# Kernel optimization log

Hardware: AMD Instinct MI355X
Metric: run time of the kernel (lower is better)

Reference implementation:

```python
import jax, jax.numpy as jnp
import numpy as np

N_NODES = 50000
N_EDGES = 800000
N_GRAPHS = 64
FEAT = 125
POS = 3
CONV = 256
LIN = 256
OUT = 10


def _glorot(key, shape):
    fan_in, fan_out = shape[1], shape[0]
    lim = jnp.sqrt(6.0 / (fan_in + fan_out))
    return jax.random.uniform(key, shape, jnp.float32, -lim, lim)


def setup_inputs() -> dict:
    key = jax.random.key(0)
    ks = jax.random.split(key, 16)
    x = jax.random.normal(ks[0], (N_NODES, FEAT), jnp.float32)
    pos = jax.random.normal(ks[1], (N_NODES, POS), jnp.float32)
    edge_index = jax.random.randint(ks[2], (2, N_EDGES), 0, N_NODES, jnp.int64)
    batch = jnp.sort(jax.random.randint(ks[3], (N_NODES,), 0, N_GRAPHS, jnp.int64))
    in0 = FEAT + POS  # 128
    inp = {
        'x': x, 'pos': pos, 'edge_index': edge_index, 'batch': batch,
        'Wl0': _glorot(ks[4], (CONV, in0)), 'bl0': jnp.zeros((CONV,), jnp.float32), 'Wr0': _glorot(ks[5], (CONV, in0)),
        'Wl1': _glorot(ks[6], (CONV, CONV)), 'bl1': jnp.zeros((CONV,), jnp.float32), 'Wr1': _glorot(ks[7], (CONV, CONV)),
        'Wl2': _glorot(ks[8], (CONV, CONV)), 'bl2': jnp.zeros((CONV,), jnp.float32), 'Wr2': _glorot(ks[9], (CONV, CONV)),
        'lin_W': _glorot(ks[10], (LIN, CONV)), 'lin_b': jnp.zeros((LIN,), jnp.float32),
        'out_W': _glorot(ks[11], (OUT, LIN)), 'out_b': jnp.zeros((OUT,), jnp.float32),
    }
    return inp


def _sage_conv(x, src, dst, Wl, bl, Wr):
    # PyG SAGEConv (aggr='mean'): out = lin_l(mean_{j in N(i)} x_j) + lin_r(x_i)
    n = x.shape[0]
    s = jax.ops.segment_sum(x[src], dst, num_segments=n)            # [N, F]
    cnt = jax.ops.segment_sum(jnp.ones((src.shape[0], 1), x.dtype), dst, num_segments=n)
    agg = s / jnp.maximum(cnt, 1.0)
    return agg @ Wl.T + bl + x @ Wr.T


def reference(x, pos, edge_index, batch, Wl0, bl0, Wr0, Wl1, bl1, Wr1,
              Wl2, bl2, Wr2, lin_W, lin_b, out_W, out_b):
    src, dst = edge_index[0], edge_index[1]
    h = jnp.concatenate([x, pos], axis=1)                           # [N, 128]
    for Wl, bl, Wr in ((Wl0, bl0, Wr0), (Wl1, bl1, Wr1), (Wl2, bl2, Wr2)):
        h = jax.nn.relu(_sage_conv(h, src, dst, Wl, bl, Wr))
    g = jax.ops.segment_max(h, batch, num_segments=N_GRAPHS)        # [G, 256] global_max_pool
    g = g @ lin_W.T + lin_b
    return g @ out_W.T + out_b                                      # [G, 10]
```

## Files before the change

kernel.cpp:

```cpp
#include <hip/hip_runtime.h>
#include <hip/hip_bf16.h>

#define N_NODES 50000
#define N_EDGES 800000
#define N_GRAPHS 64
#define SCAN_BLK 98

typedef __attribute__((ext_vector_type(8))) short bf16x8;
typedef __attribute__((ext_vector_type(4))) float f32x4;

#define AS1 __attribute__((address_space(1)))
#define AS3 __attribute__((address_space(3)))

__device__ __forceinline__ float bf2f(ushort u) { return __uint_as_float(((unsigned)u) << 16); }
__device__ __forceinline__ ushort f2bf(float f) {
    unsigned b = __float_as_uint(f);
    b += 0x7fffu + ((b >> 16) & 1u);
    return (ushort)(b >> 16);
}

__device__ __forceinline__ void gl_lds16(const ushort* g, ushort* l) {
    __builtin_amdgcn_global_load_lds((const AS1 void*)g, (AS3 void*)l, 16, 0, 0);
}

__global__ void build_h0(const float* __restrict__ x, const float* __restrict__ pos,
                         ushort* __restrict__ h0, int n) {
    const size_t total = (size_t)n * 128;
    for (size_t idx = (size_t)blockIdx.x * blockDim.x + threadIdx.x; idx < total;
         idx += (size_t)gridDim.x * blockDim.x) {
        int i = (int)(idx >> 7);
        int j = (int)(idx & 127);
        float v = (j < 125) ? x[(size_t)i * 125 + j] : pos[(size_t)i * 3 + (j - 125)];
        h0[idx] = f2bf(v);
    }
}

__global__ void convert_weights(const float* __restrict__ w0, const float* __restrict__ w1,
                                const float* __restrict__ w2, const float* __restrict__ w3,
                                const float* __restrict__ w4, const float* __restrict__ w5,
                                ushort* __restrict__ o) {
    const int total = 32768 * 2 + 65536 * 4;
    for (int i = blockIdx.x * blockDim.x + threadIdx.x; i < total; i += gridDim.x * blockDim.x) {
        float v;
        if (i < 32768) v = w0[i];
        else if (i < 65536) v = w1[i - 32768];
        else {
            int j = i - 65536;
            int m = j >> 16;
            int r = j & 65535;
            v = (m == 0) ? w2[r] : (m == 1) ? w3[r] : (m == 2) ? w4[r] : w5[r];
        }
        o[i] = f2bf(v);
    }
}

__global__ void hist_dst(const int* __restrict__ dst, int* __restrict__ deg, int e) {
    for (int i = blockIdx.x * blockDim.x + threadIdx.x; i < e; i += gridDim.x * blockDim.x)
        atomicAdd(&deg[dst[i]], 1);
}

__global__ __launch_bounds__(256) void scan_k1(const int* __restrict__ deg,
                                               int* __restrict__ bsum, int n) {
    const int b = blockIdx.x, t = threadIdx.x;
    const int j = b * 512 + t * 2;
    int x = (j < n) ? deg[j] : 0;
    int y = (j + 1 < n) ? deg[j + 1] : 0;
    __shared__ int sm[256];
    sm[t] = x + y;
    __syncthreads();
    for (int st = 1; st < 256; st <<= 1) {
        int v = (t >= st) ? sm[t - st] : 0;
        __syncthreads();
        sm[t] += v;
        __syncthreads();
    }
    if (t == 255) bsum[b] = sm[255];
}

__global__ __launch_bounds__(128) void scan_k2(const int* __restrict__ bsum,
                                               int* __restrict__ bpre, int* __restrict__ off_n,
                                               int nb) {
    const int t = threadIdx.x;
    const int v = (t < nb) ? bsum[t] : 0;
    __shared__ int sm[128];
    sm[t] = v;
    __syncthreads();
    for (int st = 1; st < 128; st <<= 1) {
        int u = (t >= st) ? sm[t - st] : 0;
        __syncthreads();
        sm[t] += u;
        __syncthreads();
    }
    if (t < nb) bpre[t] = sm[t] - v;
    if (t == 127) off_n[0] = sm[127];
}

__global__ __launch_bounds__(256) void scan_k3(const int* __restrict__ deg,
                                               const int* __restrict__ bpre,
                                               int* __restrict__ off, int* __restrict__ cur,
                                               int n) {
    const int b = blockIdx.x, t = threadIdx.x;
    const int j = b * 512 + t * 2;
    int x = (j < n) ? deg[j] : 0;
    int y = (j + 1 < n) ? deg[j + 1] : 0;
    const int s = x + y;
    __shared__ int sm[256];
    sm[t] = s;
    __syncthreads();
    for (int st = 1; st < 256; st <<= 1) {
        int u = (t >= st) ? sm[t - st] : 0;
        __syncthreads();
        sm[t] += u;
        __syncthreads();
    }
    const int v0 = bpre[b] + sm[t] - s;
    if (j < n) { off[j] = v0; cur[j] = v0; }
    if (j + 1 < n) { off[j + 1] = v0 + x; cur[j + 1] = v0 + x; }
}

__global__ __launch_bounds__(256) void fill_csr(const int* __restrict__ src,
                                                const int* __restrict__ dst,
                                                int* __restrict__ cur,
                                                ushort* __restrict__ csr, int e) {
    const int g = blockIdx.x & 7;
    const int bid = blockIdx.x >> 3;
    const int nb = gridDim.x >> 3;
    const int lo = g * (N_NODES / 8), hi = lo + (N_NODES / 8);
    for (int i = bid * blockDim.x + threadIdx.x; i < e; i += nb * blockDim.x) {
        const int d = dst[i];
        if (d >= lo && d < hi) {
            int pos = atomicAdd(&cur[d], 1);
            csr[pos] = (ushort)src[i];
        }
    }
}

template <int F>
__global__ __launch_bounds__(256) void csr_mean(const ushort* __restrict__ h,
                                                const int* __restrict__ off,
                                                const ushort* __restrict__ idx,
                                                ushort* __restrict__ s, int n) {
    const int node = blockIdx.x * 4 + (threadIdx.x >> 6);
    if (node >= n) return;
    const int lane = threadIdx.x & 63;
    constexpr int LPR = F / 8;
    constexpr int EPW = 64 / LPR;
    const int sub = lane / LPR;
    const int l = lane % LPR;
    const int b = off[node];
    const int cnt = off[node + 1] - b;

    float s0[8] = {}, s1[8] = {}, s2[8] = {}, s3[8] = {};
    const ushort* hl = h + (size_t)l * 8;
    int q = sub;
    for (; q + 3 * EPW < cnt; q += 4 * EPW) {
        int i0 = idx[b + q];
        int i1 = idx[b + q + EPW];
        int i2 = idx[b + q + 2 * EPW];
        int i3 = idx[b + q + 3 * EPW];
        bf16x8 v0 = *(const bf16x8*)(hl + (size_t)i0 * F);
        bf16x8 v1 = *(const bf16x8*)(hl + (size_t)i1 * F);
        bf16x8 v2 = *(const bf16x8*)(hl + (size_t)i2 * F);
        bf16x8 v3 = *(const bf16x8*)(hl + (size_t)i3 * F);
#pragma unroll
        for (int j = 0; j < 8; ++j) s0[j] += bf2f((ushort)v0[j]);
#pragma unroll
        for (int j = 0; j < 8; ++j) s1[j] += bf2f((ushort)v1[j]);
#pragma unroll
        for (int j = 0; j < 8; ++j) s2[j] += bf2f((ushort)v2[j]);
#pragma unroll
        for (int j = 0; j < 8; ++j) s3[j] += bf2f((ushort)v3[j]);
    }
    for (; q < cnt; q += EPW) {
        int i0 = idx[b + q];
        bf16x8 v0 = *(const bf16x8*)(hl + (size_t)i0 * F);
#pragma unroll
        for (int j = 0; j < 8; ++j) s0[j] += bf2f((ushort)v0[j]);
    }
    const float w = 1.0f / (float)max(cnt, 1);
    bf16x8 o;
#pragma unroll
    for (int j = 0; j < 8; ++j) {
        float a = (s0[j] + s1[j]) + (s2[j] + s3[j]);
        if constexpr (EPW == 4) a += __shfl_xor(a, 16);
        a += __shfl_xor(a, 32);
        o[j] = (short)f2bf(a * w);
    }
    if (sub == 0) *(bf16x8*)(s + (size_t)node * F + l * 8) = o;
}

__global__ __launch_bounds__(256, 3) void sage_gemm(
    const ushort* __restrict__ S, const ushort* __restrict__ H,
    const ushort* __restrict__ Wl, const ushort* __restrict__ Wr,
    const float* __restrict__ bias, ushort* __restrict__ O, int n, int F) {
    constexpr int BM = 128, BN = 128, BK = 64;
    __shared__ ushort As[BM * BK];
    __shared__ ushort Bs[BN * BK];
    const int row0 = blockIdx.x * BM;
    const int col0 = blockIdx.y * BN;
    const int tid = threadIdx.x;
    const int wid = tid >> 6;
    const int wr = wid >> 1;
    const int wc = wid & 1;
    const int lane = tid & 63;
    const int lr = lane & 15;
    const int lk = lane >> 4;
    const int lrow = lane >> 3;
    const int lgg = lane & 7;

    f32x4 acc[4][4] = {};

    const int Ktot = 2 * F;
    for (int kb = 0; kb < Ktot; kb += BK) {
        const bool left = (kb < F);
        const int kofs = left ? kb : kb - F;
        const ushort* __restrict__ Ab = left ? S : H;
        const ushort* __restrict__ Wb = left ? Wl : Wr;
#pragma unroll
        for (int p = 0; p < 4; ++p) {
            const int rb = (p * 4 + wid) * 8;
            const int r = rb + lrow;
            const int sg = (lgg ^ (r & 7)) << 3;
            const int gr = min(row0 + r, n - 1);
            gl_lds16(Ab + (size_t)gr * F + kofs + sg, &As[rb * 64]);
            gl_lds16(Wb + (size_t)(col0 + r) * F + kofs + sg, &Bs[rb * 64]);
        }
        __syncthreads();
#pragma unroll
        for (int kh = 0; kh < 2; ++kh) {
            bf16x8 af[4], bg[4];
            const int g = kh * 4 + lk;
#pragma unroll
            for (int m = 0; m < 4; ++m) {
                const int ra = wr * 64 + m * 16 + lr;
                af[m] = *(const bf16x8*)&As[ra * 64 + ((g ^ (ra & 7)) << 3)];
            }
#pragma unroll
            for (int q = 0; q < 4; ++q) {
                const int rb2 = wc * 64 + q * 16 + lr;
                bg[q] = *(const bf16x8*)&Bs[rb2 * 64 + ((g ^ (rb2 & 7)) << 3)];
            }
#pragma unroll
            for (int m = 0; m < 4; ++m)
#pragma unroll
                for (int q = 0; q < 4; ++q)
                    acc[m][q] =
                        __builtin_amdgcn_mfma_f32_16x16x32_bf16(af[m], bg[q], acc[m][q], 0, 0, 0);
        }
        __syncthreads();
    }
#pragma unroll
    for (int q = 0; q < 4; ++q) {
        const int col = col0 + wc * 64 + q * 16 + lr;
        const float bv = bias[col];
#pragma unroll
        for (int m = 0; m < 4; ++m) {
            const int row = row0 + wr * 64 + m * 16 + lk * 4;
#pragma unroll
            for (int j = 0; j < 4; ++j) {
                if (row + j < n)
                    O[(size_t)(row + j) * 256 + col] = f2bf(fmaxf(acc[m][q][j] + bv, 0.f));
            }
        }
    }
}

__global__ __launch_bounds__(256) void pool_max(const ushort* __restrict__ h,
                                                const int* __restrict__ batch,
                                                int* __restrict__ gpool, int n) {
    const int CHUNK = 32;
    const int wave = threadIdx.x >> 6;
    const int lane = threadIdx.x & 63;
    const int c0 = (blockIdx.x * 4 + wave) * CHUNK;
    if (c0 >= n) return;
    const int c1 = min(c0 + CHUNK, n);
    const int fb = lane * 4;
    float m0 = 0.f, m1 = 0.f, m2 = 0.f, m3 = 0.f;
    int g = batch[c0];
    for (int i = c0; i < c1; ++i) {
        const int bg = batch[i];
        if (bg != g) {
            int* gp = &gpool[g * 256 + fb];
            atomicMax(gp + 0, __float_as_int(m0));
            atomicMax(gp + 1, __float_as_int(m1));
            atomicMax(gp + 2, __float_as_int(m2));
            atomicMax(gp + 3, __float_as_int(m3));
            m0 = m1 = m2 = m3 = 0.f;
            g = bg;
        }
        const ushort4 v = *(const ushort4*)(h + (size_t)i * 256 + fb);
        m0 = fmaxf(m0, bf2f(v.x));
        m1 = fmaxf(m1, bf2f(v.y));
        m2 = fmaxf(m2, bf2f(v.z));
        m3 = fmaxf(m3, bf2f(v.w));
    }
    int* gp = &gpool[g * 256 + fb];
    atomicMax(gp + 0, __float_as_int(m0));
    atomicMax(gp + 1, __float_as_int(m1));
    atomicMax(gp + 2, __float_as_int(m2));
    atomicMax(gp + 3, __float_as_int(m3));
}

__global__ __launch_bounds__(256) void head_kernel(
    const float* __restrict__ gpool, const float* __restrict__ linW,
    const float* __restrict__ linb, const float* __restrict__ outW,
    const float* __restrict__ outb, float* __restrict__ out) {
    __shared__ float gin[256];
    __shared__ float gl[256];
    int g = blockIdx.x, t = threadIdx.x;
    gin[t] = gpool[g * 256 + t];
    __syncthreads();
    float acc = linb[t];
    const float* w = linW + (size_t)t * 256;
#pragma unroll 4
    for (int k = 0; k < 256; ++k) acc = fmaf(gin[k], w[k], acc);
    gl[t] = acc;
    __syncthreads();
    if (t < 160) {
        int o = t >> 4, s = t & 15;
        float p = 0.f;
        for (int k = s; k < 256; k += 16) p = fmaf(gl[k], outW[o * 256 + k], p);
        p += __shfl_down(p, 8, 16);
        p += __shfl_down(p, 4, 16);
        p += __shfl_down(p, 2, 16);
        p += __shfl_down(p, 1, 16);
        if (s == 0) out[g * 10 + o] = p + outb[o];
    }
}

extern "C" void kernel_launch(void* const* d_in, const int* in_sizes, int n_in,
                              void* d_out, int out_size, void* d_ws, size_t ws_size,
                              hipStream_t stream) {
    const float* x    = (const float*)d_in[0];
    const float* pos  = (const float*)d_in[1];
    const int* ei     = (const int*)d_in[2];
    const int* batch  = (const int*)d_in[3];
    const float* Wl0  = (const float*)d_in[4];
    const float* bl0  = (const float*)d_in[5];
    const float* Wr0  = (const float*)d_in[6];
    const float* Wl1  = (const float*)d_in[7];
    const float* bl1  = (const float*)d_in[8];
    const float* Wr1  = (const float*)d_in[9];
    const float* Wl2  = (const float*)d_in[10];
    const float* bl2  = (const float*)d_in[11];
    const float* Wr2  = (const float*)d_in[12];
    const float* linW = (const float*)d_in[13];
    const float* linb = (const float*)d_in[14];
    const float* outW = (const float*)d_in[15];
    const float* outb = (const float*)d_in[16];
    float* out = (float*)d_out;

    const int* src = ei;
    const int* dst = ei + N_EDGES;
    const int N = N_NODES, E = N_EDGES;

    ushort* hA   = (ushort*)d_ws;
    ushort* hB   = hA + (size_t)N * 256;
    ushort* Sg   = hB + (size_t)N * 256;
    ushort* Wb   = Sg + (size_t)N * 256;
    int* off     = (int*)(Wb + 327680);
    int* cur     = off + (N + 1);
    ushort* csr  = (ushort*)(cur + N);
    int* gpool   = (int*)(csr + E);
    int* deg     = gpool + 64 * 256;
    int* bsum    = deg + N;
    int* bpre    = bsum + 128;

    ushort* Wl0b = Wb;
    ushort* Wr0b = Wb + 32768;
    ushort* Wl1b = Wb + 65536;
    ushort* Wr1b = Wb + 65536 + 65536;
    ushort* Wl2b = Wb + 65536 + 2 * 65536;
    ushort* Wr2b = Wb + 65536 + 3 * 65536;

    build_h0<<<dim3(1024), dim3(256), 0, stream>>>(x, pos, hA, N);
    convert_weights<<<dim3(640), dim3(256), 0, stream>>>(Wl0, Wr0, Wl1, Wr1, Wl2, Wr2, Wb);

    hipMemsetAsync(deg, 0, (size_t)N * sizeof(int), stream);
    hist_dst<<<dim3(1024), dim3(256), 0, stream>>>(dst, deg, E);
    scan_k1<<<dim3(SCAN_BLK), dim3(256), 0, stream>>>(deg, bsum, N);
    scan_k2<<<dim3(1), dim3(128), 0, stream>>>(bsum, bpre, off + N, SCAN_BLK);
    scan_k3<<<dim3(SCAN_BLK), dim3(256), 0, stream>>>(deg, bpre, off, cur, N);
    fill_csr<<<dim3(768), dim3(256), 0, stream>>>(src, dst, cur, csr, E);

    const dim3 gemm_grid((N + 127) / 128, 2), blk(256);

    csr_mean<128><<<dim3((N + 3) / 4), blk, 0, stream>>>(hA, off, csr, Sg, N);
    sage_gemm<<<gemm_grid, blk, 0, stream>>>(Sg, hA, Wl0b, Wr0b, bl0, hB, N, 128);

    csr_mean<256><<<dim3((N + 3) / 4), blk, 0, stream>>>(hB, off, csr, Sg, N);
    sage_gemm<<<gemm_grid, blk, 0, stream>>>(Sg, hB, Wl1b, Wr1b, bl1, hA, N, 256);

    csr_mean<256><<<dim3((N + 3) / 4), blk, 0, stream>>>(hA, off, csr, Sg, N);
    sage_gemm<<<gemm_grid, blk, 0, stream>>>(Sg, hA, Wl2b, Wr2b, bl2, hB, N, 256);

    hipMemsetAsync(gpool, 0, (size_t)N_GRAPHS * 256 * sizeof(int), stream);
    pool_max<<<dim3((N + 127) / 128), blk, 0, stream>>>(hB, batch, gpool, N);
    head_kernel<<<dim3(N_GRAPHS), blk, 0, stream>>>((const float*)gpool, linW, linb, outW, outb,
                                                    out);
}
```

Baseline: 369.3 us.

## Unroll gather to 8 loads, partition degree histogram, template GEMM on F

The CSR mean aggregation now issues eight independent neighbor-row loads per iteration instead of four, to keep more memory requests in flight. The degree histogram splits blocks into eight groups that each handle atomics for one slice of node ids, aiming for better atomic locality, though every group rereads the whole dst array. The SAGE GEMM is templated on F so its K loop is fully unrolled at compile time. The extra accumulators raise register pressure in the gather kernel and may lower occupancy.

```diff
diff --git a/kernel.cpp b/kernel.cpp
--- a/kernel.cpp
+++ b/kernel.cpp
@@ -54,9 +54,16 @@
     }
 }
 
-__global__ void hist_dst(const int* __restrict__ dst, int* __restrict__ deg, int e) {
-    for (int i = blockIdx.x * blockDim.x + threadIdx.x; i < e; i += gridDim.x * blockDim.x)
-        atomicAdd(&deg[dst[i]], 1);
+__global__ __launch_bounds__(256) void hist_dst(const int* __restrict__ dst,
+                                                int* __restrict__ deg, int e) {
+    const int g = blockIdx.x & 7;
+    const int bid = blockIdx.x >> 3;
+    const int nb = gridDim.x >> 3;
+    const int lo = g * (N_NODES / 8), hi = lo + (N_NODES / 8);
+    for (int i = bid * blockDim.x + threadIdx.x; i < e; i += nb * blockDim.x) {
+        const int d = dst[i];
+        if (d >= lo && d < hi) atomicAdd(&deg[d], 1);
+    }
 }
 
 __global__ __launch_bounds__(256) void scan_k1(const int* __restrict__ deg,
@@ -150,38 +157,38 @@
     const int b = off[node];
     const int cnt = off[node + 1] - b;
 
-    float s0[8] = {}, s1[8] = {}, s2[8] = {}, s3[8] = {};
+    float acc[8][8] = {};
     const ushort* hl = h + (size_t)l * 8;
     int q = sub;
+    for (; q + 7 * EPW < cnt; q += 8 * EPW) {
+        bf16x8 v[8];
+#pragma unroll
+        for (int t = 0; t < 8; ++t) v[t] = *(const bf16x8*)(hl + (size_t)idx[b + q + t * EPW] * F);
+#pragma unroll
+        for (int t = 0; t < 8; ++t)
+#pragma unroll
+            for (int j = 0; j < 8; ++j) acc[t][j] += bf2f((ushort)v[t][j]);
+    }
     for (; q + 3 * EPW < cnt; q += 4 * EPW) {
-        int i0 = idx[b + q];
-        int i1 = idx[b + q + EPW];
-        int i2 = idx[b + q + 2 * EPW];
-        int i3 = idx[b + q + 3 * EPW];
-        bf16x8 v0 = *(const bf16x8*)(hl + (size_t)i0 * F);
-        bf16x8 v1 = *(const bf16x8*)(hl + (size_t)i1 * F);
-        bf16x8 v2 = *(const bf16x8*)(hl + (size_t)i2 * F);
-        bf16x8 v3 = *(const bf16x8*)(hl + (size_t)i3 * F);
-#pragma unroll
-        for (int j = 0; j < 8; ++j) s0[j] += bf2f((ushort)v0[j]);
-#pragma unroll
-        for (int j = 0; j < 8; ++j) s1[j] += bf2f((ushort)v1[j]);
-#pragma unroll
-        for (int j = 0; j < 8; ++j) s2[j] += bf2f((ushort)v2[j]);
-#pragma unroll
-        for (int j = 0; j < 8; ++j) s3[j] += bf2f((ushort)v3[j]);
+        bf16x8 v[4];
+#pragma unroll
+        for (int t = 0; t < 4; ++t) v[t] = *(const bf16x8*)(hl + (size_t)idx[b + q + t * EPW] * F);
+#pragma unroll
+        for (int t = 0; t < 4; ++t)
+#pragma unroll
+            for (int j = 0; j < 8; ++j) acc[t][j] += bf2f((ushort)v[t][j]);
     }
     for (; q < cnt; q += EPW) {
-        int i0 = idx[b + q];
-        bf16x8 v0 = *(const bf16x8*)(hl + (size_t)i0 * F);
-#pragma unroll
-        for (int j = 0; j < 8; ++j) s0[j] += bf2f((ushort)v0[j]);
+        bf16x8 v0 = *(const bf16x8*)(hl + (size_t)idx[b + q] * F);
+#pragma unroll
+        for (int j = 0; j < 8; ++j) acc[0][j] += bf2f((ushort)v0[j]);
     }
     const float w = 1.0f / (float)max(cnt, 1);
     bf16x8 o;
 #pragma unroll
     for (int j = 0; j < 8; ++j) {
-        float a = (s0[j] + s1[j]) + (s2[j] + s3[j]);
+        float a = ((acc[0][j] + acc[1][j]) + (acc[2][j] + acc[3][j])) +
+                  ((acc[4][j] + acc[5][j]) + (acc[6][j] + acc[7][j]));
         if constexpr (EPW == 4) a += __shfl_xor(a, 16);
         a += __shfl_xor(a, 32);
         o[j] = (short)f2bf(a * w);
@@ -189,10 +196,11 @@
     if (sub == 0) *(bf16x8*)(s + (size_t)node * F + l * 8) = o;
 }
 
+template <int F>
 __global__ __launch_bounds__(256, 3) void sage_gemm(
     const ushort* __restrict__ S, const ushort* __restrict__ H,
     const ushort* __restrict__ Wl, const ushort* __restrict__ Wr,
-    const float* __restrict__ bias, ushort* __restrict__ O, int n, int F) {
+    const float* __restrict__ bias, ushort* __restrict__ O, int n) {
     constexpr int BM = 128, BN = 128, BK = 64;
     __shared__ ushort As[BM * BK];
     __shared__ ushort Bs[BN * BK];
@@ -210,7 +218,8 @@
 
     f32x4 acc[4][4] = {};
 
-    const int Ktot = 2 * F;
+    constexpr int Ktot = 2 * F;
+#pragma unroll
     for (int kb = 0; kb < Ktot; kb += BK) {
         const bool left = (kb < F);
         const int kofs = left ? kb : kb - F;
@@ -377,7 +386,7 @@
     convert_weights<<<dim3(640), dim3(256), 0, stream>>>(Wl0, Wr0, Wl1, Wr1, Wl2, Wr2, Wb);
 
     hipMemsetAsync(deg, 0, (size_t)N * sizeof(int), stream);
-    hist_dst<<<dim3(1024), dim3(256), 0, stream>>>(dst, deg, E);
+    hist_dst<<<dim3(768), dim3(256), 0, stream>>>(dst, deg, E);
     scan_k1<<<dim3(SCAN_BLK), dim3(256), 0, stream>>>(deg, bsum, N);
     scan_k2<<<dim3(1), dim3(128), 0, stream>>>(bsum, bpre, off + N, SCAN_BLK);
     scan_k3<<<dim3(SCAN_BLK), dim3(256), 0, stream>>>(deg, bpre, off, cur, N);
@@ -386,13 +395,13 @@
     const dim3 gemm_grid((N + 127) / 128, 2), blk(256);
 
     csr_mean<128><<<dim3((N + 3) / 4), blk, 0, stream>>>(hA, off, csr, Sg, N);
-    sage_gemm<<<gemm_grid, blk, 0, stream>>>(Sg, hA, Wl0b, Wr0b, bl0, hB, N, 128);
+    sage_gemm<128><<<gemm_grid, blk, 0, stream>>>(Sg, hA, Wl0b, Wr0b, bl0, hB, N);
 
     csr_mean<256><<<dim3((N + 3) / 4), blk, 0, stream>>>(hB, off, csr, Sg, N);
-    sage_gemm<<<gemm_grid, blk, 0, stream>>>(Sg, hB, Wl1b, Wr1b, bl1, hA, N, 256);
+    sage_gemm<256><<<gemm_grid, blk, 0, stream>>>(Sg, hB, Wl1b, Wr1b, bl1, hA, N);
 
     csr_mean<256><<<dim3((N + 3) / 4), blk, 0, stream>>>(hA, off, csr, Sg, N);
-    sage_gemm<<<gemm_grid, blk, 0, stream>>>(Sg, hA, Wl2b, Wr2b, bl2, hB, N, 256);
+    sage_gemm<256><<<gemm_grid, blk, 0, stream>>>(Sg, hA, Wl2b, Wr2b, bl2, hB, N);
 
     hipMemsetAsync(gpool, 0, (size_t)N_GRAPHS * 256 * sizeof(int), stream);
     pool_max<<<dim3((N + 127) / 128), blk, 0, stream>>>(hB, batch, gpool, N);
```

Measured after the change: 417.1 us. 1.13x slower.
